# Kernel optimization log

Hardware: AMD Instinct MI355X
Metric: run time of the kernel (lower is better)

Reference implementation:

```python
import jax, jax.numpy as jnp
import numpy as np

N = 100000   # nodes
E = 1600000  # edges (avg degree 16)
D_IN = 48
D_OUT = 16


def setup_inputs() -> dict:
    key = jax.random.key(0)
    k0, k1, k2, k3 = jax.random.split(key, 4)
    x = jax.random.normal(k0, (N, D_IN), dtype=jnp.float32)
    edge_index = jax.random.randint(k1, (2, E), 0, N, dtype=jnp.int32)
    scale = 1.0 / np.sqrt(D_IN)
    W_mu = jax.random.normal(k2, (D_IN, D_OUT), dtype=jnp.float32) * scale
    W_logstd = jax.random.normal(k3, (D_IN, D_OUT), dtype=jnp.float32) * scale
    b_mu = jnp.zeros((D_OUT,), dtype=jnp.float32)
    b_logstd = jnp.zeros((D_OUT,), dtype=jnp.float32)
    return {"x": x, "edge_index": edge_index, "W_mu": W_mu, "b_mu": b_mu,
            "W_logstd": W_logstd, "b_logstd": b_logstd}


def _gcn_aggregate(x, edge_index):
    """Shared GCN propagation: D^-1/2 (A + I) D^-1/2 x, done ONCE for both convs.

    Matches PyG GCNConv defaults (add_self_loops=True, normalize=True).
    """
    src, dst = edge_index[0], edge_index[1]
    n = x.shape[0]
    # degree with self-loops: 1 + in-degree (counted on dst, edge weight 1)
    deg = jnp.ones((n,), x.dtype).at[dst].add(jnp.float32(1.0))
    dinv = jax.lax.rsqrt(deg)                      # deg^-1/2, [N]
    norm = dinv[src] * dinv[dst]                   # per-edge norm, [E]
    # neighbor aggregation (gather -> scale -> scatter-add)
    agg = jax.ops.segment_sum(norm[:, None] * x[src], dst, num_segments=n)
    # self-loop term: deg^-1 * x_i
    agg = agg + x * (dinv * dinv)[:, None]
    return agg


def reference(x, edge_index, W_mu, b_mu, W_logstd, b_logstd):
    agg = _gcn_aggregate(x, edge_index)            # [N, D_IN], shared pass
    mu = agg @ W_mu + b_mu                         # [N, D_OUT]
    logstd = agg @ W_logstd + b_logstd             # [N, D_OUT]
    return (mu, logstd)
```

## Files before the change

kernel.cpp:

```cpp
#include <hip/hip_runtime.h>

#define DIN 48
#define DOUT 16
#define DC 32
#define BSH 7
#define BNODES 128
#define NBP 1024
#define EPB 8192
#define TPB_BIN 1024
#define CAPB 4096
#define XS 49

typedef unsigned int uint;
typedef unsigned short ushort;

__device__ __forceinline__ float b2f(ushort u) {
    union { uint i; float f; } v; v.i = ((uint)u) << 16; return v.f;
}
__device__ __forceinline__ ushort f2b(float f) {
    union { float f; uint i; } v; v.f = f;
    uint b = v.i;
    return (ushort)((b + 0x7FFFu + ((b >> 16) & 1u)) >> 16);
}


__global__ __launch_bounds__(TPB_BIN) void k_bin2(
        const int* __restrict__ src, const int* __restrict__ dst,
        int* __restrict__ bfill, uint* __restrict__ ebuf, int e_cnt, int nb) {
    __shared__ uint stageV[EPB];
    __shared__ ushort stageB[EPB];
    __shared__ int hist[NBP];
    __shared__ int lofs[NBP];
    __shared__ int gbase[NBP];

    int t = threadIdx.x;
    int e0 = blockIdx.x * EPB;
    int ec = min(EPB, e_cnt - e0);

    hist[t] = 0;
    __syncthreads();
    for (int k = t; k < ec; k += TPB_BIN) atomicAdd(&hist[dst[e0 + k] >> BSH], 1);
    __syncthreads();
    {
        int v = hist[t];
        uint* sd = stageV;
        sd[t] = (uint)v;
        __syncthreads();
#pragma unroll
        for (int off = 1; off < NBP; off <<= 1) {
            uint x = (t >= off) ? sd[t - off] : 0u;
            __syncthreads();
            sd[t] += x;
            __syncthreads();
        }
        lofs[t] = (int)sd[t] - v;
    }
    if (t < nb) {
        int h = hist[t];
        if (h > 0) gbase[t] = atomicAdd(&bfill[t], h);
    }
    __syncthreads();
    hist[t] = 0;
    __syncthreads();
    for (int k = t; k < ec; k += TPB_BIN) {
        int d = dst[e0 + k], s = src[e0 + k];
        int b = d >> BSH;
        int p = atomicAdd(&hist[b], 1);
        int idx = lofs[b] + p;
        stageV[idx] = ((uint)(d & (BNODES - 1)) << 17) | (uint)s;
        stageB[idx] = (ushort)b;
    }
    __syncthreads();
    for (int i = t; i < ec; i += TPB_BIN) {
        int b = stageB[i];
        int off = gbase[b] + (i - lofs[b]);
        if (off < CAPB) ebuf[(size_t)b * CAPB + off] = stageV[i];
    }
}


struct SortStage { uint in[CAPB]; int out[CAPB]; };
union SmemU { SortStage s; float xl[BNODES * XS]; };

__global__ __launch_bounds__(256) void k_sortproj(
        const uint* __restrict__ ebuf, const int* __restrict__ bfill,
        const float* __restrict__ x,
        const float* __restrict__ Wmu, const float* __restrict__ Wls,
        uint* __restrict__ nodeinfo, int* __restrict__ esrc,
        float* __restrict__ dinv, ushort* __restrict__ projh, int n, int nb) {
    __shared__ SmemU u;
    __shared__ float Wl[DIN * DC];
    __shared__ int cntl[BNODES], lofs[BNODES], fill[BNODES], sc[BNODES];
    __shared__ float dvl[BNODES];

    int b = blockIdx.x, t = threadIdx.x;
    int base = b << BSH;

    for (int idx = t; idx < DIN * DC; idx += 256) {
        int k = idx >> 5, j = idx & 31;
        Wl[idx] = (j < DOUT) ? Wmu[k * DOUT + j] : Wls[k * DOUT + (j - DOUT)];
    }

    int m = min(bfill[b], CAPB);

    if (t < BNODES) { cntl[t] = 0; fill[t] = 0; }
    __syncthreads();

    for (int i = t; i < m; i += 256) {
        uint pk = ebuf[(size_t)b * CAPB + i];
        u.s.in[i] = pk;
        atomicAdd(&cntl[pk >> 17], 1);
    }
    __syncthreads();

    if (t < BNODES) sc[t] = cntl[t];
    __syncthreads();
#pragma unroll
    for (int off = 1; off < BNODES; off <<= 1) {
        int v = (t < BNODES && t >= off) ? sc[t - off] : 0;
        __syncthreads();
        if (t < BNODES) sc[t] += v;
        __syncthreads();
    }
    if (t < BNODES) {
        int lo = sc[t] - cntl[t];
        lofs[t] = lo;
        int d = base + t;
        if (d < n) {
            nodeinfo[d] = (uint)lo | ((uint)cntl[t] << 13);
            float dv = rsqrtf(1.0f + (float)cntl[t]);
            dinv[d] = dv;
            dvl[t] = dv;
        }
    }
    __syncthreads();

    for (int i = t; i < m; i += 256) {
        uint pk = u.s.in[i];
        int ln = (int)(pk >> 17);
        int s = (int)(pk & 0x1FFFFu);
        int r = atomicAdd(&fill[ln], 1);
        u.s.out[lofs[ln] + r] = s;
    }
    __syncthreads();

    for (int i = t; i < m; i += 256) esrc[(size_t)b * CAPB + i] = u.s.out[i];
    __syncthreads();

#pragma unroll
    for (int it = 0; it < 6; ++it) {
        int f4 = t + 256 * it;
        int fb = f4 * 4;
        int node = fb / DIN, k = fb % DIN;
        int g = base + node;
        if (g < n) {
            float4 v = *reinterpret_cast<const float4*>(x + (size_t)g * DIN + k);
            float* p = &u.xl[node * XS + k];
            p[0] = v.x; p[1] = v.y; p[2] = v.z; p[3] = v.w;
        }
    }
    __syncthreads();

    int nc = t & 7;
    int nr = t >> 3;
    int c0 = nc * 4;

    float4 acc[4];
#pragma unroll
    for (int q = 0; q < 4; ++q) acc[q] = make_float4(0.f, 0.f, 0.f, 0.f);

#pragma unroll 4
    for (int k = 0; k < DIN; ++k) {
        float4 w = *reinterpret_cast<const float4*>(&Wl[k * DC + c0]);
#pragma unroll
        for (int q = 0; q < 4; ++q) {
            float xv = u.xl[(nr * 4 + q) * XS + k];
            acc[q].x += xv * w.x;
            acc[q].y += xv * w.y;
            acc[q].z += xv * w.z;
            acc[q].w += xv * w.w;
        }
    }

#pragma unroll
    for (int q = 0; q < 4; ++q) {
        int ln = nr * 4 + q;
        int d = base + ln;
        if (d >= n) continue;
        float dv = dvl[ln];
        ushort4 ph;
        ph.x = f2b(dv * acc[q].x); ph.y = f2b(dv * acc[q].y);
        ph.z = f2b(dv * acc[q].z); ph.w = f2b(dv * acc[q].w);
        *reinterpret_cast<ushort4*>(projh + ((size_t)d << 5) + c0) = ph;
    }
}


__global__ __launch_bounds__(256) void k_agg5(
        const int* __restrict__ esrc, const uint* __restrict__ nodeinfo,
        const float* __restrict__ dinv, const ushort* __restrict__ projh,
        const float* __restrict__ bmu, const float* __restrict__ bls,
        float* __restrict__ out, int n) {
    int t = threadIdx.x;
    int l = t & 7;
    int g = t >> 3;
    int d = blockIdx.x * 32 + g;
    if (d >= n) return;
    uint info = nodeinfo[d];
    int start = (d >> BSH) * CAPB + (int)(info & 0x1FFFu);
    int end = start + (int)(info >> 13);
    int c0 = l * 4;

    float4 acc;
    {
        ushort4 s4 = *reinterpret_cast<const ushort4*>(projh + ((size_t)d << 5) + c0);
        acc.x = b2f(s4.x); acc.y = b2f(s4.y); acc.z = b2f(s4.z); acc.w = b2f(s4.w);
    }

    int k = start;
    for (; k + 8 <= end; k += 8) {
        ushort4 p[8];
#pragma unroll
        for (int u2 = 0; u2 < 8; ++u2) {
            int s = esrc[k + u2];
            p[u2] = *reinterpret_cast<const ushort4*>(projh + ((size_t)s << 5) + c0);
        }
#pragma unroll
        for (int u2 = 0; u2 < 8; ++u2) {
            acc.x += b2f(p[u2].x); acc.y += b2f(p[u2].y);
            acc.z += b2f(p[u2].z); acc.w += b2f(p[u2].w);
        }
    }
    for (; k < end; ++k) {
        int s = esrc[k];
        ushort4 pv = *reinterpret_cast<const ushort4*>(projh + ((size_t)s << 5) + c0);
        acc.x += b2f(pv.x); acc.y += b2f(pv.y); acc.z += b2f(pv.z); acc.w += b2f(pv.w);
    }

    float dv = dinv[d];
    float4 bias = (l < 4) ? *reinterpret_cast<const float4*>(bmu + c0)
                          : *reinterpret_cast<const float4*>(bls + (c0 - DOUT));
    float4 ov;
    ov.x = bias.x + dv * acc.x; ov.y = bias.y + dv * acc.y;
    ov.z = bias.z + dv * acc.z; ov.w = bias.w + dv * acc.w;
    float* o = (l < 4) ? (out + (size_t)d * DOUT + c0)
                       : (out + (size_t)n * DOUT + (size_t)d * DOUT + (c0 - DOUT));
    *reinterpret_cast<float4*>(o) = ov;
}


__global__ void k_init_deg(float* __restrict__ deg, int n) {
    int i = blockIdx.x * blockDim.x + threadIdx.x;
    if (i < n) deg[i] = 1.0f;
}

__global__ void k_count(const int* __restrict__ dst, float* __restrict__ deg, int e_cnt) {
    int e = blockIdx.x * blockDim.x + threadIdx.x;
    if (e < e_cnt) unsafeAtomicAdd(&deg[dst[e]], 1.0f);
}

__global__ void k_projF(const float* __restrict__ x,
                        const float* __restrict__ Wmu, const float* __restrict__ bmu,
                        const float* __restrict__ Wls, const float* __restrict__ bls,
                        float* __restrict__ deg_dinv, float* __restrict__ proj,
                        float* __restrict__ out, int n) {
    __shared__ float Ws[DIN * DC];
    __shared__ float bs[DC];
    int t = threadIdx.x;
    for (int idx = t; idx < DIN * DC; idx += blockDim.x) {
        int k = idx >> 5, j = idx & 31;
        Ws[idx] = (j < DOUT) ? Wmu[k * DOUT + j] : Wls[k * DOUT + (j - DOUT)];
    }
    if (t < DC) bs[t] = (t < DOUT) ? bmu[t] : bls[t - DOUT];
    __syncthreads();
    int i = blockIdx.x * blockDim.x + t;
    if (i >= n) return;
    float xr[DIN];
    const float4* xp = reinterpret_cast<const float4*>(x + (size_t)i * DIN);
#pragma unroll
    for (int q = 0; q < DIN / 4; ++q) {
        float4 v = xp[q];
        xr[4 * q + 0] = v.x; xr[4 * q + 1] = v.y;
        xr[4 * q + 2] = v.z; xr[4 * q + 3] = v.w;
    }
    float acc[DC];
#pragma unroll
    for (int j = 0; j < DC; ++j) acc[j] = 0.0f;
#pragma unroll 4
    for (int k = 0; k < DIN; ++k) {
        float xv = xr[k];
#pragma unroll
        for (int j = 0; j < DC; ++j) acc[j] += xv * Ws[k * DC + j];
    }
    float dv = rsqrtf(deg_dinv[i]);
    deg_dinv[i] = dv;
    float d2 = dv * dv;
    float4* pp = reinterpret_cast<float4*>(proj + (size_t)i * DC);
#pragma unroll
    for (int q = 0; q < DC / 4; ++q) {
        float4 v;
        v.x = acc[4 * q + 0]; v.y = acc[4 * q + 1];
        v.z = acc[4 * q + 2]; v.w = acc[4 * q + 3];
        pp[q] = v;
    }
    float* omu = out + (size_t)i * DOUT;
    float* ols = out + (size_t)n * DOUT + (size_t)i * DOUT;
#pragma unroll
    for (int j = 0; j < DOUT; ++j) omu[j] = bs[j] + d2 * acc[j];
#pragma unroll
    for (int j = 0; j < DOUT; ++j) ols[j] = bs[DOUT + j] + d2 * acc[DOUT + j];
}

__global__ void k_scatterF(const int* __restrict__ src, const int* __restrict__ dst,
                           const float* __restrict__ dinv, const float* __restrict__ proj,
                           float* __restrict__ out, int e_cnt, int n) {
    long long gid = (long long)blockIdx.x * blockDim.x + threadIdx.x;
    int e = (int)(gid >> 5);
    int j = (int)(gid & 31);
    if (e >= e_cnt) return;
    int s = src[e], d = dst[e];
    float norm = dinv[s] * dinv[d];
    float v = norm * proj[(size_t)s * DC + j];
    float* o = (j < DOUT) ? (out + (size_t)d * DOUT + j)
                          : (out + (size_t)n * DOUT + (size_t)d * DOUT + (j - DOUT));
    unsafeAtomicAdd(o, v);
}


extern "C" void kernel_launch(void* const* d_in, const int* in_sizes, int n_in,
                              void* d_out, int out_size, void* d_ws, size_t ws_size,
                              hipStream_t stream) {
    const float* x   = (const float*)d_in[0];
    const int*   ei  = (const int*)d_in[1];
    const float* Wmu = (const float*)d_in[2];
    const float* bmu = (const float*)d_in[3];
    const float* Wls = (const float*)d_in[4];
    const float* bls = (const float*)d_in[5];
    float* out = (float*)d_out;

    int n = in_sizes[0] / DIN;
    int e_cnt = in_sizes[1] / 2;
    const int* src = ei;
    const int* dst = ei + e_cnt;

    int nb = (n + BNODES - 1) >> BSH;
    bool pack_ok = (n <= (1 << 17));

    size_t need = (size_t)NBP * 4
                + (size_t)n * 4
                + (size_t)n * 4
                + (size_t)nb * CAPB * 4
                + (size_t)nb * CAPB * 4
                + (size_t)n * DC * 2;

    int nblk = (n + 255) / 256;
    int eblk = (e_cnt + 255) / 256;

    if (nb <= NBP && pack_ok && ws_size >= need) {
        char* w = (char*)d_ws;
        int*    bfill = (int*)w;     w += NBP * 4;
        float*  dinv  = (float*)w;   w += (size_t)n * 4;
        uint*   ninfo = (uint*)w;    w += (size_t)n * 4;
        uint*   ebuf  = (uint*)w;    w += (size_t)nb * CAPB * 4;
        int*    esrc  = (int*)w;     w += (size_t)nb * CAPB * 4;
        ushort* projh = (ushort*)w;

        hipMemsetAsync(bfill, 0, NBP * sizeof(int), stream);
        int binblk = (e_cnt + EPB - 1) / EPB;
        k_bin2<<<binblk, TPB_BIN, 0, stream>>>(src, dst, bfill, ebuf, e_cnt, nb);
        k_sortproj<<<nb, 256, 0, stream>>>(ebuf, bfill, x, Wmu, Wls,
                                           ninfo, esrc, dinv, projh, n, nb);
        k_agg5<<<(n + 31) / 32, 256, 0, stream>>>(esrc, ninfo, dinv, projh,
                                                  bmu, bls, out, n);
    } else {
        float* deg  = (float*)d_ws;
        float* proj = deg + n;
        k_init_deg<<<nblk, 256, 0, stream>>>(deg, n);
        k_count<<<eblk, 256, 0, stream>>>(dst, deg, e_cnt);
        k_projF<<<nblk, 256, 0, stream>>>(x, Wmu, bmu, Wls, bls, deg, proj, out, n);
        long long tasks = (long long)e_cnt * DC;
        k_scatterF<<<(int)((tasks + 255) / 256), 256, 0, stream>>>(src, dst, deg, proj, out, e_cnt, n);
    }
}
```

Measured before the change: 74.11 us.

## Cache edge loads in registers, prefetch x early, and software-pipeline esrc loads

In the binning kernel, each thread now loads its src/dst edges once into registers during the histogram pass and reuses them in the scatter pass, so the second global read of the edge lists goes away. The sort/projection kernel issues its x row loads at kernel start so they overlap the sorting phase. The aggregation kernel prefetches the next 8 esrc indices while gathering the current batch, which shortens the dependent load chain. These changes raise register pressure, which may reduce occupancy, especially in the 1024-thread binning kernel.

```diff
diff --git a/kernel.cpp b/kernel.cpp
--- a/kernel.cpp
+++ b/kernel.cpp
@@ -39,7 +39,19 @@
 
     hist[t] = 0;
     __syncthreads();
-    for (int k = t; k < ec; k += TPB_BIN) atomicAdd(&hist[dst[e0 + k] >> BSH], 1);
+
+    uint pv[8]; ushort pb[8];
+#pragma unroll
+    for (int it = 0; it < 8; ++it) {
+        int k = t + TPB_BIN * it;
+        if (k < ec) {
+            int d = dst[e0 + k], s = src[e0 + k];
+            int b = d >> BSH;
+            pv[it] = ((uint)(d & (BNODES - 1)) << 17) | (uint)s;
+            pb[it] = (ushort)b;
+            atomicAdd(&hist[b], 1);
+        }
+    }
     __syncthreads();
     {
         int v = hist[t];
@@ -62,13 +74,16 @@
     __syncthreads();
     hist[t] = 0;
     __syncthreads();
-    for (int k = t; k < ec; k += TPB_BIN) {
-        int d = dst[e0 + k], s = src[e0 + k];
-        int b = d >> BSH;
-        int p = atomicAdd(&hist[b], 1);
-        int idx = lofs[b] + p;
-        stageV[idx] = ((uint)(d & (BNODES - 1)) << 17) | (uint)s;
-        stageB[idx] = (ushort)b;
+#pragma unroll
+    for (int it = 0; it < 8; ++it) {
+        int k = t + TPB_BIN * it;
+        if (k < ec) {
+            int b = pb[it];
+            int p = atomicAdd(&hist[b], 1);
+            int idx = lofs[b] + p;
+            stageV[idx] = pv[it];
+            stageB[idx] = pb[it];
+        }
     }
     __syncthreads();
     for (int i = t; i < ec; i += TPB_BIN) {
@@ -96,6 +111,16 @@
     int b = blockIdx.x, t = threadIdx.x;
     int base = b << BSH;
 
+    float4 xr[6];
+#pragma unroll
+    for (int it = 0; it < 6; ++it) {
+        int f4 = t + 256 * it;
+        int fb = f4 * 4;
+        int node = fb / DIN, k2 = fb % DIN;
+        int g = base + node;
+        if (g < n) xr[it] = *reinterpret_cast<const float4*>(x + (size_t)g * DIN + k2);
+    }
+
     for (int idx = t; idx < DIN * DC; idx += 256) {
         int k = idx >> 5, j = idx & 31;
         Wl[idx] = (j < DOUT) ? Wmu[k * DOUT + j] : Wls[k * DOUT + (j - DOUT)];
@@ -151,12 +176,11 @@
     for (int it = 0; it < 6; ++it) {
         int f4 = t + 256 * it;
         int fb = f4 * 4;
-        int node = fb / DIN, k = fb % DIN;
+        int node = fb / DIN, k2 = fb % DIN;
         int g = base + node;
         if (g < n) {
-            float4 v = *reinterpret_cast<const float4*>(x + (size_t)g * DIN + k);
-            float* p = &u.xl[node * XS + k];
-            p[0] = v.x; p[1] = v.y; p[2] = v.z; p[3] = v.w;
+            float* p = &u.xl[node * XS + k2];
+            p[0] = xr[it].x; p[1] = xr[it].y; p[2] = xr[it].z; p[3] = xr[it].w;
         }
     }
     __syncthreads();
@@ -218,18 +242,30 @@
     }
 
     int k = start;
-    for (; k + 8 <= end; k += 8) {
+    int nxt[8];
+    if (k + 8 <= end) {
+#pragma unroll
+        for (int u2 = 0; u2 < 8; ++u2) nxt[u2] = esrc[k + u2];
+    }
+    while (k + 8 <= end) {
+        int cur[8];
+#pragma unroll
+        for (int u2 = 0; u2 < 8; ++u2) cur[u2] = nxt[u2];
+        int k2 = k + 8;
+        if (k2 + 8 <= end) {
+#pragma unroll
+            for (int u2 = 0; u2 < 8; ++u2) nxt[u2] = esrc[k2 + u2];
+        }
         ushort4 p[8];
 #pragma unroll
-        for (int u2 = 0; u2 < 8; ++u2) {
-            int s = esrc[k + u2];
-            p[u2] = *reinterpret_cast<const ushort4*>(projh + ((size_t)s << 5) + c0);
-        }
+        for (int u2 = 0; u2 < 8; ++u2)
+            p[u2] = *reinterpret_cast<const ushort4*>(projh + ((size_t)cur[u2] << 5) + c0);
 #pragma unroll
         for (int u2 = 0; u2 < 8; ++u2) {
             acc.x += b2f(p[u2].x); acc.y += b2f(p[u2].y);
             acc.z += b2f(p[u2].z); acc.w += b2f(p[u2].w);
         }
+        k = k2;
     }
     for (; k < end; ++k) {
         int s = esrc[k];
```

Result: faster. 70.93 us (-4.3%).
